# Kernel optimization log

Measured on AMD Instinct MI355X. Metric: run time of the kernel, lower is better.

Reference implementation:

```python
import jax, jax.numpy as jnp
import numpy as np
import math

NUM_HEADS = 16
ROPE_BASE = 10000.0
SLIDING_WINDOW = 512  # note: original triu-then-tril composition makes the mask empty (no-op)


def _rope_cos_sin(seq_len, head_dim, dtype):
    inv_freq = 1.0 / (ROPE_BASE ** (jnp.arange(0, head_dim, 2, dtype=jnp.float32) / head_dim))
    t = jnp.arange(seq_len, dtype=jnp.float32)
    freqs = t[:, None] * inv_freq[None, :]          # [S, D/2]
    emb = jnp.concatenate([freqs, freqs], axis=-1)  # [S, D]
    # reshape to broadcast over [B, S, H, D]
    return jnp.cos(emb)[None, :, None, :].astype(dtype), jnp.sin(emb)[None, :, None, :].astype(dtype)


def _rotate_half(x):
    x1, x2 = jnp.split(x, 2, axis=-1)
    return jnp.concatenate([-x2, x1], axis=-1)


def setup_inputs() -> dict:
    key = jax.random.key(0)
    ks = jax.random.split(key, 9)
    B, S, E = 2, 2048, 2048
    sc = 1.0 / math.sqrt(E)
    return {
        "hidden_states": jax.random.normal(ks[0], (B, S, E), dtype=jnp.float32),
        "Wq": jax.random.normal(ks[1], (E, E), dtype=jnp.float32) * sc,
        "bq": jax.random.normal(ks[2], (E,), dtype=jnp.float32) * 0.01,
        "Wk": jax.random.normal(ks[3], (E, E), dtype=jnp.float32) * sc,
        "bk": jax.random.normal(ks[4], (E,), dtype=jnp.float32) * 0.01,
        "Wv": jax.random.normal(ks[5], (E, E), dtype=jnp.float32) * sc,
        "bv": jax.random.normal(ks[6], (E,), dtype=jnp.float32) * 0.01,
        "Wo": jax.random.normal(ks[7], (E, E), dtype=jnp.float32) * sc,
        "bo": jax.random.normal(ks[8], (E,), dtype=jnp.float32) * 0.01,
    }


def reference(hidden_states, Wq, bq, Wk, bk, Wv, bv, Wo, bo):
    B, S, E = hidden_states.shape
    H = NUM_HEADS
    D = E // H
    q = (hidden_states @ Wq.T + bq).reshape(B, S, H, D)
    k = (hidden_states @ Wk.T + bk).reshape(B, S, H, D)
    v = (hidden_states @ Wv.T + bv).reshape(B, S, H, D)

    cos, sin = _rope_cos_sin(S, D, q.dtype)
    q = q * cos + _rotate_half(q) * sin
    k = k * cos + _rotate_half(k) * sin

    scale = 1.0 / math.sqrt(D)
    scores = jnp.einsum("bqhd,bkhd->bhqk", q, k) * scale  # [B,H,S,S]
    # Faithful to source: triu(ones, +w) followed by tril(..., -w) is empty -> mask is a no-op.
    attn = jax.nn.softmax(scores, axis=-1)
    out = jnp.einsum("bhqk,bkhd->bqhd", attn, v).reshape(B, S, E)
    return out @ Wo.T + bo
```

## Files before the change

### kernel.cpp

```cpp
#include <hip/hip_runtime.h>
#include <hip/hip_bf16.h>

#define B_ 2
#define S_ 2048
#define E_ 2048
#define H_ 16
#define D_ 128
#define M_ (B_*S_)
#define NQKV_ (3*E_)

typedef __attribute__((ext_vector_type(8))) short bf16x8;
typedef __attribute__((ext_vector_type(4))) float f32x4;
typedef __attribute__((ext_vector_type(4))) unsigned short u16x4;
typedef __attribute__((ext_vector_type(2))) unsigned u32x2;

__device__ __forceinline__ unsigned short f2bf(float f) {
  union { float f; unsigned u; } v; v.f = f;
  unsigned r = v.u + 0x7fffu + ((v.u >> 16) & 1u);
  return (unsigned short)(r >> 16);
}
__device__ __forceinline__ float bf2f(unsigned short h) {
  union { unsigned u; float f; } v; v.u = ((unsigned)h) << 16;
  return v.f;
}

__device__ __forceinline__ void gload_lds16(const void* g, void* l) {
  __builtin_amdgcn_global_load_lds(
      (const __attribute__((address_space(1))) unsigned*)g,
      (__attribute__((address_space(3))) unsigned*)l, 16, 0, 0);
}

__global__ __launch_bounds__(256) void prep_kernel(
    const float* __restrict__ hs,
    const float* __restrict__ Wq, const float* __restrict__ Wk, const float* __restrict__ Wv,
    const float* __restrict__ Wo,
    const float* __restrict__ bq, const float* __restrict__ bk, const float* __restrict__ bv,
    unsigned short* __restrict__ hsb, unsigned short* __restrict__ Wqkv,
    unsigned short* __restrict__ Wob, float* __restrict__ biasqkv,
    float* __restrict__ cosT, float* __restrict__ sinT)
{
  const int seg = blockIdx.y;
  const int t0 = blockIdx.x * 256 + threadIdx.x;
  const int stride = gridDim.x * 256;
  if (seg == 0) {
    const int n = (M_*E_)/4;
    for (int i = t0; i < n; i += stride) {
      f32x4 v = ((const f32x4*)hs)[i];
      u16x4 o; o[0]=f2bf(v[0]); o[1]=f2bf(v[1]); o[2]=f2bf(v[2]); o[3]=f2bf(v[3]);
      ((u16x4*)hsb)[i] = o;
    }
  } else if (seg == 1) {
    const int n = (3*E_*E_)/4;
    for (int i = t0; i < n; i += stride) {
      int e4 = i << 2;
      int r = e4 >> 11;
      int k = e4 & 2047;
      const float* src = (r < E_) ? (Wq + ((size_t)r << 11) + k)
                       : (r < 2*E_) ? (Wk + ((size_t)(r - E_) << 11) + k)
                       : (Wv + ((size_t)(r - 2*E_) << 11) + k);
      f32x4 v = *(const f32x4*)src;
      u16x4 o; o[0]=f2bf(v[0]); o[1]=f2bf(v[1]); o[2]=f2bf(v[2]); o[3]=f2bf(v[3]);
      ((u16x4*)Wqkv)[i] = o;
    }
  } else if (seg == 2) {
    const int n = (E_*E_)/4;
    for (int i = t0; i < n; i += stride) {
      f32x4 v = ((const f32x4*)Wo)[i];
      u16x4 o; o[0]=f2bf(v[0]); o[1]=f2bf(v[1]); o[2]=f2bf(v[2]); o[3]=f2bf(v[3]);
      ((u16x4*)Wob)[i] = o;
    }
  } else if (seg == 3) {
    for (int i = t0; i < NQKV_; i += stride)
      biasqkv[i] = (i < E_) ? bq[i] : (i < 2*E_) ? bk[i - E_] : bv[i - 2*E_];
  } else {
    for (int i = t0; i < S_*64; i += stride) {
      int j = i & 63, s = i >> 6;
      float inv = exp2f(-(float)j * (13.287712379549449f / 64.0f));
      float ang = (float)s * inv;
      cosT[i] = cosf(ang);
      sinT[i] = sinf(ang);
    }
  }
}

#define STAGE8(basePtr, BUF, AB, KS, KT) do { \
    unsigned short* dst_ = lds + (BUF)*32768 + (AB)*16384 + (KS)*8192; \
    const unsigned short* src_ = (basePtr) + (KT)*64 + (KS)*32; \
    _Pragma("unroll") \
    for (int j_ = 0; j_ < 2; ++j_) { \
      int cc_ = (j_ << 9) + tid; \
      int row_ = cc_ >> 2, c2_ = cc_ & 3; \
      int sc_ = c2_ ^ ((row_ >> 1) & 3); \
      gload_lds16(src_ + (size_t)row_*K + sc_*8, (char*)dst_ + cc_*16); \
    } } while(0)

#define LOADA8(MH, KS, BUF) do { \
    const unsigned short* Ab_ = lds + (BUF)*32768 + (KS)*8192; \
    _Pragma("unroll") \
    for (int j_ = 0; j_ < 4; ++j_) { \
      int row_ = wr*128 + ((MH)*4 + j_)*16 + l15; \
      af[j_] = *(const bf16x8*)(Ab_ + row_*32 + ((l4 ^ ((row_>>1)&3)) << 3)); \
    } } while(0)

#define LOADB8(KS, BUF) do { \
    const unsigned short* Bb_ = lds + (BUF)*32768 + 16384 + (KS)*8192; \
    _Pragma("unroll") \
    for (int j_ = 0; j_ < 4; ++j_) { \
      int row_ = wc*64 + j_*16 + l15; \
      bf[j_] = *(const bf16x8*)(Bb_ + row_*32 + ((l4 ^ ((row_>>1)&3)) << 3)); \
    } } while(0)

#define MFMAQ8(MH) do { \
    _Pragma("unroll") \
    for (int mm_ = 0; mm_ < 4; ++mm_) \
      _Pragma("unroll") \
      for (int nn_ = 0; nn_ < 4; ++nn_) \
        acc[(MH)*4+mm_][nn_] = __builtin_amdgcn_mfma_f32_16x16x32_bf16(af[mm_], bf[nn_], acc[(MH)*4+mm_][nn_], 0,0,0); \
    } while(0)

#define VMW6 do { if (nl) asm volatile("s_waitcnt vmcnt(6)" ::: "memory"); \
                  else    asm volatile("s_waitcnt vmcnt(0)" ::: "memory"); } while(0)
#define VMNONE do {} while(0)

#define PHASE8(MH, KS, BUF, ISSUE, WAITV) do { \
    LOADA8(MH, KS, BUF); \
    if ((MH) == 0) LOADB8(KS, BUF); \
    ISSUE; \
    __builtin_amdgcn_sched_barrier(0); \
    __builtin_amdgcn_s_barrier(); \
    asm volatile("s_waitcnt lgkmcnt(0)" ::: "memory"); \
    __builtin_amdgcn_sched_barrier(0); \
    __builtin_amdgcn_s_setprio(1); \
    MFMAQ8(MH); \
    __builtin_amdgcn_s_setprio(0); \
    __builtin_amdgcn_sched_barrier(0); \
    WAITV; \
    __builtin_amdgcn_s_barrier(); \
  } while(0)

__global__ __launch_bounds__(512, 2) void gemm8(
    const unsigned short* __restrict__ A,
    const unsigned short* __restrict__ Bm,
    const float* __restrict__ bias,
    unsigned short* __restrict__ Cv,
    int M, int N, int K)
{
  __shared__ __align__(16) unsigned short lds[65536];
  const int tid = threadIdx.x;
  const int lane = tid & 63;
  const int w = tid >> 6;
  const int wr = w >> 2, wc = w & 3;
  const int l15 = lane & 15, l4 = lane >> 4;

  const int ntile = N >> 8;
  int wg = blockIdx.x;
  const int cpx = gridDim.x >> 3;
  wg = (wg & 7) * cpx + (wg >> 3);
  const int tm = wg / ntile, tn = wg % ntile;

  const unsigned short* Abase = A + ((size_t)tm*256)*K;
  const unsigned short* Bbase = Bm + ((size_t)tn*256)*K;

  f32x4 acc[8][4] = {};
  bf16x8 af[4], bf[4];

  const int NITER = K >> 7;

  STAGE8(Bbase, 0, 1, 0, 0); STAGE8(Abase, 0, 0, 0, 0);
  STAGE8(Bbase, 0, 1, 1, 0); STAGE8(Abase, 0, 0, 1, 0);
  STAGE8(Bbase, 1, 1, 0, 1); STAGE8(Abase, 1, 0, 0, 1);
  STAGE8(Bbase, 1, 1, 1, 1);
  __builtin_amdgcn_sched_barrier(0);
  asm volatile("s_waitcnt vmcnt(6)" ::: "memory");
  __builtin_amdgcn_s_barrier();

  for (int i = 0; i < NITER; ++i) {
    const int t1k = 2*i + 1, t2k = 2*i + 2, t3k = 2*i + 3;
    const bool nl = (i < NITER - 1);
    PHASE8(0, 0, 0, STAGE8(Abase, 1, 0, 1, t1k), VMNONE);
    PHASE8(1, 0, 0, if (nl) STAGE8(Bbase, 0, 1, 0, t2k), VMNONE);
    PHASE8(0, 1, 0, if (nl) STAGE8(Abase, 0, 0, 0, t2k), VMNONE);
    PHASE8(1, 1, 0, if (nl) STAGE8(Bbase, 0, 1, 1, t2k), VMW6);
    PHASE8(0, 0, 1, if (nl) STAGE8(Abase, 0, 0, 1, t2k), VMNONE);
    PHASE8(1, 0, 1, if (nl) STAGE8(Bbase, 1, 1, 0, t3k), VMNONE);
    PHASE8(0, 1, 1, if (nl) STAGE8(Abase, 1, 0, 0, t3k), VMNONE);
    PHASE8(1, 1, 1, if (nl) STAGE8(Bbase, 1, 1, 1, t3k), VMW6);
  }

  #pragma unroll
  for (int mt = 0; mt < 8; ++mt) {
    #pragma unroll
    for (int nt = 0; nt < 4; ++nt) {
      int colg = tn*256 + wc*64 + nt*16 + l15;
      float bvv = bias[colg];
      #pragma unroll
      for (int r = 0; r < 4; ++r) {
        int rowg = tm*256 + wr*128 + mt*16 + l4*4 + r;
        Cv[(size_t)rowg*N + colg] = f2bf(acc[mt][nt][r] + bvv);
      }
    }
  }
}

template<int OUT_F32>
__global__ __launch_bounds__(256) void gemm_bt(
    const unsigned short* __restrict__ A,
    const unsigned short* __restrict__ Bm,
    const float* __restrict__ bias,
    void* __restrict__ Cv,
    int M, int N, int K)
{
  __shared__ unsigned short lA[128*64];
  __shared__ unsigned short lB[128*64];
  const int tid = threadIdx.x;
  const int lane = tid & 63;
  const int w = tid >> 6;
  const int wr = w >> 1, wc = w & 1;
  const int ntile = N >> 7;
  const int tm = blockIdx.x / ntile, tn = blockIdx.x % ntile;
  const int l15 = lane & 15, l4 = lane >> 4;

  f32x4 acc[4][4] = {};

  for (int kt = 0; kt < K; kt += 64) {
    #pragma unroll
    for (int i = 0; i < 4; ++i) {
      int cc = i*256 + tid;
      int row = cc >> 3, col = cc & 7;
      int scol = col ^ (row & 7);
      gload_lds16(A + (size_t)(tm*128 + row)*K + kt + scol*8, (char*)lA + cc*16);
    }
    #pragma unroll
    for (int i = 0; i < 4; ++i) {
      int cc = i*256 + tid;
      int row = cc >> 3, col = cc & 7;
      int scol = col ^ (row & 7);
      gload_lds16(Bm + (size_t)(tn*128 + row)*K + kt + scol*8, (char*)lB + cc*16);
    }
    asm volatile("s_waitcnt vmcnt(0)" ::: "memory");
    __syncthreads();

    #pragma unroll
    for (int ks = 0; ks < 2; ++ks) {
      bf16x8 af[4], bfr[4];
      #pragma unroll
      for (int mt = 0; mt < 4; ++mt) {
        int row = wr*64 + mt*16 + l15;
        int ch = (ks*4 + l4) ^ (row & 7);
        af[mt] = *(const bf16x8*)(lA + row*64 + ch*8);
      }
      #pragma unroll
      for (int nt = 0; nt < 4; ++nt) {
        int row = wc*64 + nt*16 + l15;
        int ch = (ks*4 + l4) ^ (row & 7);
        bfr[nt] = *(const bf16x8*)(lB + row*64 + ch*8);
      }
      #pragma unroll
      for (int mt = 0; mt < 4; ++mt)
        #pragma unroll
        for (int nt = 0; nt < 4; ++nt)
          acc[mt][nt] = __builtin_amdgcn_mfma_f32_16x16x32_bf16(af[mt], bfr[nt], acc[mt][nt], 0, 0, 0);
    }
    __syncthreads();
  }

  #pragma unroll
  for (int mt = 0; mt < 4; ++mt) {
    #pragma unroll
    for (int nt = 0; nt < 4; ++nt) {
      int colg = tn*128 + wc*64 + nt*16 + l15;
      float bvv = bias[colg];
      #pragma unroll
      for (int r = 0; r < 4; ++r) {
        int rowg = tm*128 + wr*64 + mt*16 + l4*4 + r;
        float v = acc[mt][nt][r] + bvv;
        if (OUT_F32) ((float*)Cv)[(size_t)rowg*N + colg] = v;
        else ((unsigned short*)Cv)[(size_t)rowg*N + colg] = f2bf(v);
      }
    }
  }
}

__global__ __launch_bounds__(256) void rope_kernel(
    unsigned short* __restrict__ qkv, const float* __restrict__ cosT, const float* __restrict__ sinT)
{
  int t = blockIdx.x*256 + threadIdx.x;
  int i  = t & 63;
  int h  = (t >> 6) & 15;
  int m  = t >> 10;
  int s  = m & (S_-1);
  float c = cosT[s*64 + i], sn = sinT[s*64 + i];
  const float scale = 0.08838834764831845f * 1.4426950408889634f;
  size_t base = (size_t)m*NQKV_ + h*128;
  float q1 = bf2f(qkv[base+i]), q2 = bf2f(qkv[base+64+i]);
  qkv[base+i]    = f2bf((q1*c - q2*sn)*scale);
  qkv[base+64+i] = f2bf((q2*c + q1*sn)*scale);
  size_t kb = base + E_;
  float k1 = bf2f(qkv[kb+i]), k2 = bf2f(qkv[kb+64+i]);
  qkv[kb+i]    = f2bf(k1*c - k2*sn);
  qkv[kb+64+i] = f2bf(k2*c + k1*sn);
}

__global__ __launch_bounds__(256) void transv_kernel(
    const unsigned short* __restrict__ qkv, unsigned short* __restrict__ Vt)
{
  __shared__ unsigned short t[32][33];
  int bid = blockIdx.x;
  int st = bid & 63;
  int dt = (bid >> 6) & 3;
  int bh = bid >> 8;
  int b = bh >> 4, h = bh & 15;
  int tx = threadIdx.x & 31, ty = threadIdx.x >> 5;
  #pragma unroll
  for (int j = 0; j < 4; ++j) {
    int r = ty + j*8;
    t[r][tx] = qkv[(size_t)(b*S_ + st*32 + r)*NQKV_ + 2*E_ + h*128 + dt*32 + tx];
  }
  __syncthreads();
  #pragma unroll
  for (int j = 0; j < 4; ++j) {
    int r = ty + j*8;
    Vt[((size_t)bh*D_ + dt*32 + r)*S_ + st*32 + tx] = t[tx][r];
  }
}

__global__ __launch_bounds__(256, 4) void attn_kernel(
    const unsigned short* __restrict__ qkv, const unsigned short* __restrict__ Vt,
    unsigned short* __restrict__ Ao)
{
  __shared__ unsigned short lK[64*128];
  __shared__ unsigned short lV[128*64];
  __shared__ __align__(16) unsigned short lP[4*16*64];
  const int bid = blockIdx.x;
  const int qt = bid & 31;
  const int bh = bid >> 5;
  const int b = bh >> 4, h = bh & 15;
  const int tid = threadIdx.x, lane = tid & 63, w = tid >> 6;
  const int l15 = lane & 15, l4 = lane >> 4;

  const int qrow = qt*64 + w*16 + l15;
  const unsigned short* qp = qkv + (size_t)(b*S_ + qrow)*NQKV_ + h*128 + l4*8;
  bf16x8 qf[4];
  #pragma unroll
  for (int f = 0; f < 4; ++f) qf[f] = *(const bf16x8*)(qp + f*32);

  f32x4 O[8];
  #pragma unroll
  for (int i = 0; i < 8; ++i) O[i] = (f32x4){0.f,0.f,0.f,0.f};
  float m = -1e30f, lsum = 0.f;

  unsigned short* myP = lP + w*(16*64);
  const int ksw = (l15 & 7) << 3;
  const size_t kbase = (size_t)b*S_*NQKV_ + E_ + (size_t)h*128;
  const size_t vbase = (size_t)bh*D_*S_;

  for (int kt = 0; kt < S_; kt += 64) {
    #pragma unroll
    for (int i = 0; i < 4; ++i) {
      int cc = i*256 + tid;
      int row = cc >> 4, col = cc & 15;
      int scol = col ^ (row & 7);
      gload_lds16(qkv + kbase + (size_t)(kt + row)*NQKV_ + scol*8, (char*)lK + cc*16);
    }
    #pragma unroll
    for (int i = 0; i < 4; ++i) {
      int cc = i*256 + tid;
      int row = cc >> 3, col = cc & 7;
      int scol = col ^ ((row & 7) ^ ((row >> 3) & 7));
      gload_lds16(Vt + vbase + (size_t)row*S_ + kt + scol*8, (char*)lV + cc*16);
    }
    asm volatile("s_waitcnt vmcnt(0)" ::: "memory");
    __syncthreads();

    f32x4 sfr[4];
    #pragma unroll
    for (int nf = 0; nf < 4; ++nf) {
      f32x4 s = (f32x4){0.f,0.f,0.f,0.f};
      #pragma unroll
      for (int ks = 0; ks < 4; ++ks) {
        int row = nf*16 + l15;
        int ch = (ks*4 + l4) ^ (row & 7);
        bf16x8 kf = *(const bf16x8*)(lK + row*128 + ch*8);
        s = __builtin_amdgcn_mfma_f32_16x16x32_bf16(kf, qf[ks], s, 0, 0, 0);
      }
      sfr[nf] = s;
    }

    float vmax = -1e30f;
    #pragma unroll
    for (int nf = 0; nf < 4; ++nf)
      #pragma unroll
      for (int r = 0; r < 4; ++r) vmax = fmaxf(vmax, sfr[nf][r]);
    vmax = fmaxf(vmax, __shfl_xor(vmax, 16, 64));
    vmax = fmaxf(vmax, __shfl_xor(vmax, 32, 64));

    if (__any(vmax > m + 8.0f)) {
      float mn = fmaxf(m, vmax);
      float al = __builtin_amdgcn_exp2f(m - mn);
      m = mn;
      lsum *= al;
      #pragma unroll
      for (int r = 0; r < 4; ++r) {
        float ar = __shfl(al, (lane & 48) + l4*4 + r, 64);
        #pragma unroll
        for (int df = 0; df < 8; ++df) O[df][r] *= ar;
      }
    }

    float ps = 0.f;
    #pragma unroll
    for (int nf = 0; nf < 4; ++nf) {
      #pragma unroll
      for (int r = 0; r < 4; ++r) {
        float p = __builtin_amdgcn_exp2f(sfr[nf][r] - m);
        sfr[nf][r] = p;
        ps += p;
      }
    }
    ps += __shfl_xor(ps, 16, 64);
    ps += __shfl_xor(ps, 32, 64);
    lsum += ps;

    #pragma unroll
    for (int nf = 0; nf < 4; ++nf) {
      unsigned lo = (unsigned)f2bf(sfr[nf][0]) | ((unsigned)f2bf(sfr[nf][1]) << 16);
      unsigned hi = (unsigned)f2bf(sfr[nf][2]) | ((unsigned)f2bf(sfr[nf][3]) << 16);
      int k0 = (nf*16 + l4*4) ^ ksw;
      u32x2 val; val[0] = lo; val[1] = hi;
      *(u32x2*)(myP + l15*64 + k0) = val;
    }
    asm volatile("s_waitcnt lgkmcnt(0)" ::: "memory");

    #pragma unroll
    for (int ks2 = 0; ks2 < 2; ++ks2) {
      int kk = (ks2*32 + l4*8) ^ ksw;
      bf16x8 pf = *(const bf16x8*)(myP + l15*64 + kk);
      #pragma unroll
      for (int df = 0; df < 8; ++df) {
        int row = df*16 + l15;
        int ch = (ks2*4 + l4) ^ ((row & 7) ^ ((row >> 3) & 7));
        bf16x8 vf = *(const bf16x8*)(lV + row*64 + ch*8);
        O[df] = __builtin_amdgcn_mfma_f32_16x16x32_bf16(pf, vf, O[df], 0, 0, 0);
      }
    }
    __syncthreads();
  }

  float linv = 1.0f / lsum;
  float inv[4];
  #pragma unroll
  for (int r = 0; r < 4; ++r) inv[r] = __shfl(linv, (lane & 48) + l4*4 + r, 64);
  #pragma unroll
  for (int df = 0; df < 8; ++df) {
    int colg = h*128 + df*16 + l15;
    #pragma unroll
    for (int r = 0; r < 4; ++r) {
      int rowg = qt*64 + w*16 + l4*4 + r;
      Ao[(size_t)(b*S_ + rowg)*E_ + colg] = f2bf(O[df][r] * inv[r]);
    }
  }
}

extern "C" void kernel_launch(void* const* d_in, const int* in_sizes, int n_in,
                              void* d_out, int out_size, void* d_ws, size_t ws_size,
                              hipStream_t stream) {
  const float* hs = (const float*)d_in[0];
  const float* Wq = (const float*)d_in[1];
  const float* bq = (const float*)d_in[2];
  const float* Wk = (const float*)d_in[3];
  const float* bk = (const float*)d_in[4];
  const float* Wv = (const float*)d_in[5];
  const float* bv = (const float*)d_in[6];
  const float* Wo = (const float*)d_in[7];
  const float* bo = (const float*)d_in[8];
  float* out = (float*)d_out;

  char* p = (char*)d_ws;
  auto alloc = [&](size_t bytes) { char* r = p; p += (bytes + 255) & ~(size_t)255; return r; };
  unsigned short* hsb  = (unsigned short*)alloc((size_t)M_*E_*2);
  unsigned short* Wqkv = (unsigned short*)alloc((size_t)NQKV_*E_*2);
  unsigned short* Wob  = (unsigned short*)alloc((size_t)E_*E_*2);
  unsigned short* qkv  = (unsigned short*)alloc((size_t)M_*NQKV_*2);
  unsigned short* Vt   = (unsigned short*)alloc((size_t)B_*H_*D_*S_*2);
  unsigned short* Ao   = (unsigned short*)alloc((size_t)M_*E_*2);
  float* biasqkv = (float*)alloc((size_t)NQKV_*4);
  float* cosT = (float*)alloc((size_t)S_*64*4);
  float* sinT = (float*)alloc((size_t)S_*64*4);

  prep_kernel<<<dim3(2048, 5), 256, 0, stream>>>(hs, Wq, Wk, Wv, Wo, bq, bk, bv,
      hsb, Wqkv, Wob, biasqkv, cosT, sinT);
  gemm8<<<dim3((M_/256)*(NQKV_/256)), 512, 0, stream>>>(hsb, Wqkv, biasqkv, qkv, M_, NQKV_, E_);
  rope_kernel<<<dim3((M_*H_*64)/256), 256, 0, stream>>>(qkv, cosT, sinT);
  transv_kernel<<<dim3(B_*H_*(D_/32)*(S_/32)), 256, 0, stream>>>(qkv, Vt);
  attn_kernel<<<dim3(B_*H_*(S_/64)), 256, 0, stream>>>(qkv, Vt, Ao);
  gemm_bt<1><<<dim3((M_/128)*(E_/128)), 256, 0, stream>>>(Ao, Wob, bo, out, M_, E_, E_);
}
```

Before: 319.0 us.

## Double-buffer LDS fragment registers to overlap LDS reads with MFMA in gemm8

Replaces the per-phase load, barrier, wait and MFMA sequence with a software pipeline using two register sets for the A and B fragments. LDS reads for the next sub-tile are issued before the current MFMA block, and the explicit lgkmcnt(0) wait and one barrier per phase are dropped. The aim is to hide LDS latency behind MFMA work and halve the barrier count. In exchange it uses more VGPRs, which could strain the 2-blocks-per-CU launch bound, and correctness now depends on the compiler inserting the right LDS waits and on barrier ordering against the overwrite of staged buffers.

New measurement: 318.1 us. No clear change (-0.3%).

```diff
diff --git a/kernel.cpp b/kernel.cpp
--- a/kernel.cpp
+++ b/kernel.cpp
@@ -94,48 +94,36 @@
       gload_lds16(src_ + (size_t)row_*K + sc_*8, (char*)dst_ + cc_*16); \
     } } while(0)
 
-#define LOADA8(MH, KS, BUF) do { \
+#define LOADA8(DST, MH, KS, BUF) do { \
     const unsigned short* Ab_ = lds + (BUF)*32768 + (KS)*8192; \
     _Pragma("unroll") \
     for (int j_ = 0; j_ < 4; ++j_) { \
       int row_ = wr*128 + ((MH)*4 + j_)*16 + l15; \
-      af[j_] = *(const bf16x8*)(Ab_ + row_*32 + ((l4 ^ ((row_>>1)&3)) << 3)); \
+      DST[j_] = *(const bf16x8*)(Ab_ + row_*32 + ((l4 ^ ((row_>>1)&3)) << 3)); \
     } } while(0)
 
-#define LOADB8(KS, BUF) do { \
+#define LOADB8(DST, KS, BUF) do { \
     const unsigned short* Bb_ = lds + (BUF)*32768 + 16384 + (KS)*8192; \
     _Pragma("unroll") \
     for (int j_ = 0; j_ < 4; ++j_) { \
       int row_ = wc*64 + j_*16 + l15; \
-      bf[j_] = *(const bf16x8*)(Bb_ + row_*32 + ((l4 ^ ((row_>>1)&3)) << 3)); \
+      DST[j_] = *(const bf16x8*)(Bb_ + row_*32 + ((l4 ^ ((row_>>1)&3)) << 3)); \
     } } while(0)
 
-#define MFMAQ8(MH) do { \
+#define PRIO_MFMA(MH, AF, BF) do { \
+    __builtin_amdgcn_s_setprio(1); \
     _Pragma("unroll") \
     for (int mm_ = 0; mm_ < 4; ++mm_) \
       _Pragma("unroll") \
       for (int nn_ = 0; nn_ < 4; ++nn_) \
-        acc[(MH)*4+mm_][nn_] = __builtin_amdgcn_mfma_f32_16x16x32_bf16(af[mm_], bf[nn_], acc[(MH)*4+mm_][nn_], 0,0,0); \
-    } while(0)
-
-#define VMW6 do { if (nl) asm volatile("s_waitcnt vmcnt(6)" ::: "memory"); \
-                  else    asm volatile("s_waitcnt vmcnt(0)" ::: "memory"); } while(0)
-#define VMNONE do {} while(0)
-
-#define PHASE8(MH, KS, BUF, ISSUE, WAITV) do { \
-    LOADA8(MH, KS, BUF); \
-    if ((MH) == 0) LOADB8(KS, BUF); \
-    ISSUE; \
+        acc[(MH)*4+mm_][nn_] = __builtin_amdgcn_mfma_f32_16x16x32_bf16(AF[mm_], BF[nn_], acc[(MH)*4+mm_][nn_], 0,0,0); \
+    __builtin_amdgcn_s_setprio(0); \
+  } while(0)
+
+#define BARPIN do { \
     __builtin_amdgcn_sched_barrier(0); \
     __builtin_amdgcn_s_barrier(); \
-    asm volatile("s_waitcnt lgkmcnt(0)" ::: "memory"); \
     __builtin_amdgcn_sched_barrier(0); \
-    __builtin_amdgcn_s_setprio(1); \
-    MFMAQ8(MH); \
-    __builtin_amdgcn_s_setprio(0); \
-    __builtin_amdgcn_sched_barrier(0); \
-    WAITV; \
-    __builtin_amdgcn_s_barrier(); \
   } while(0)
 
 __global__ __launch_bounds__(512, 2) void gemm8(
@@ -162,7 +150,7 @@
   const unsigned short* Bbase = Bm + ((size_t)tn*256)*K;
 
   f32x4 acc[8][4] = {};
-  bf16x8 af[4], bf[4];
+  bf16x8 afA[4], afB[4], bfA[4], bfB[4];
 
   const int NITER = K >> 7;
 
@@ -173,18 +161,51 @@
   __builtin_amdgcn_sched_barrier(0);
   asm volatile("s_waitcnt vmcnt(6)" ::: "memory");
   __builtin_amdgcn_s_barrier();
+  __builtin_amdgcn_sched_barrier(0);
 
   for (int i = 0; i < NITER; ++i) {
     const int t1k = 2*i + 1, t2k = 2*i + 2, t3k = 2*i + 3;
     const bool nl = (i < NITER - 1);
-    PHASE8(0, 0, 0, STAGE8(Abase, 1, 0, 1, t1k), VMNONE);
-    PHASE8(1, 0, 0, if (nl) STAGE8(Bbase, 0, 1, 0, t2k), VMNONE);
-    PHASE8(0, 1, 0, if (nl) STAGE8(Abase, 0, 0, 0, t2k), VMNONE);
-    PHASE8(1, 1, 0, if (nl) STAGE8(Bbase, 0, 1, 1, t2k), VMW6);
-    PHASE8(0, 0, 1, if (nl) STAGE8(Abase, 0, 0, 1, t2k), VMNONE);
-    PHASE8(1, 0, 1, if (nl) STAGE8(Bbase, 1, 1, 0, t3k), VMNONE);
-    PHASE8(0, 1, 1, if (nl) STAGE8(Abase, 1, 0, 0, t3k), VMNONE);
-    PHASE8(1, 1, 1, if (nl) STAGE8(Bbase, 1, 1, 1, t3k), VMW6);
+    STAGE8(Abase, 1, 0, 1, t1k);
+    LOADA8(afA, 0, 0, 0); LOADB8(bfA, 0, 0);
+    LOADA8(afB, 1, 0, 0);
+    PRIO_MFMA(0, afA, bfA);
+    BARPIN;
+    if (nl) STAGE8(Bbase, 0, 1, 0, t2k);
+    LOADA8(afA, 0, 1, 0); LOADB8(bfB, 1, 0);
+    PRIO_MFMA(1, afB, bfA);
+    BARPIN;
+    if (nl) STAGE8(Abase, 0, 0, 0, t2k);
+    LOADA8(afB, 1, 1, 0);
+    PRIO_MFMA(0, afA, bfB);
+    BARPIN;
+    if (nl) STAGE8(Bbase, 0, 1, 1, t2k);
+    PRIO_MFMA(1, afB, bfB);
+    __builtin_amdgcn_sched_barrier(0);
+    if (nl) asm volatile("s_waitcnt vmcnt(6)" ::: "memory");
+    else    asm volatile("s_waitcnt vmcnt(0)" ::: "memory");
+    __builtin_amdgcn_s_barrier();
+    __builtin_amdgcn_sched_barrier(0);
+    if (nl) STAGE8(Abase, 0, 0, 1, t2k);
+    LOADA8(afA, 0, 0, 1); LOADB8(bfA, 0, 1);
+    LOADA8(afB, 1, 0, 1);
+    PRIO_MFMA(0, afA, bfA);
+    BARPIN;
+    if (nl) STAGE8(Bbase, 1, 1, 0, t3k);
+    LOADA8(afA, 0, 1, 1); LOADB8(bfB, 1, 1);
+    PRIO_MFMA(1, afB, bfA);
+    BARPIN;
+    if (nl) STAGE8(Abase, 1, 0, 0, t3k);
+    LOADA8(afB, 1, 1, 1);
+    PRIO_MFMA(0, afA, bfB);
+    BARPIN;
+    if (nl) STAGE8(Bbase, 1, 1, 1, t3k);
+    PRIO_MFMA(1, afB, bfB);
+    __builtin_amdgcn_sched_barrier(0);
+    if (nl) asm volatile("s_waitcnt vmcnt(6)" ::: "memory");
+    else    asm volatile("s_waitcnt vmcnt(0)" ::: "memory");
+    __builtin_amdgcn_s_barrier();
+    __builtin_amdgcn_sched_barrier(0);
   }
 
   #pragma unroll
```
